# Performance work log

Hardware: AMD Instinct MI355X
Metric: run time of the kernel (lower is better)

The kernel has to match this reference:

```python
import jax, jax.numpy as jnp
import numpy as np

CH = 512


def _maxpool2(t):
    # 2x2 max pool, stride 2, NCHW
    B, C, H, W = t.shape
    return t.reshape(B, C, H // 2, 2, W // 2, 2).max(axis=(3, 5))


def setup_inputs() -> dict:
    key = jax.random.key(0)
    ks = jax.random.split(key, 6)
    B, C, H, W = 8, CH, 64, 64
    x = jax.random.normal(ks[0], (B, C, H, W), dtype=jnp.float32)
    # 1x1 conv weights stored as [out_ch, in_ch]
    w_theta = jax.random.normal(ks[1], (C // 8, C), dtype=jnp.float32) * (1.0 / np.sqrt(C))
    w_phi = jax.random.normal(ks[2], (C // 8, C), dtype=jnp.float32) * (1.0 / np.sqrt(C))
    w_g = jax.random.normal(ks[3], (C // 2, C), dtype=jnp.float32) * (1.0 / np.sqrt(C))
    w_o = jax.random.normal(ks[4], (C, C // 2), dtype=jnp.float32) * (1.0 / np.sqrt(C // 2))
    # gamma is a learned scalar (init 0.0 in the original); use 0.5 so the
    # attention branch contributes to the output for testing purposes.
    gamma = jnp.float32(0.5)
    return {"x": x, "w_theta": w_theta, "w_phi": w_phi, "w_g": w_g, "w_o": w_o, "gamma": gamma}


def reference(x, w_theta, w_phi, w_g, w_o, gamma):
    B, C, H, W = x.shape
    c8, c2 = C // 8, C // 2
    # 1x1 conv projections
    theta = jnp.einsum('bchw,oc->bohw', x, w_theta)           # [B, C/8, H, W]
    phi = _maxpool2(jnp.einsum('bchw,oc->bohw', x, w_phi))    # [B, C/8, H/2, W/2]
    g = _maxpool2(jnp.einsum('bchw,oc->bohw', x, w_g))        # [B, C/2, H/2, W/2]
    n, m = H * W, (H * W) // 4
    theta = theta.reshape(B, c8, n)
    phi = phi.reshape(B, c8, m)
    g = g.reshape(B, c2, m)
    # unscaled attention scores: [B, n, m]
    beta = jax.nn.softmax(jnp.einsum('bcn,bcm->bnm', theta, phi), axis=-1)
    # attend: g @ beta^T -> [B, C/2, n]
    att = jnp.einsum('bcm,bnm->bcn', g, beta).reshape(B, c2, H, W)
    o = jnp.einsum('bchw,oc->bohw', att, w_o)                 # [B, C, H, W]
    return gamma * o + x
```

## Files before the change

kernel.cpp:

```cpp
#include <hip/hip_runtime.h>
#include <math.h>

constexpr int CB = 8;
constexpr int CC = 512;
constexpr int CN = 4096;
constexpr int CM = 1024;
constexpr int C8 = 64;
constexpr int C2 = 256;

typedef __attribute__((ext_vector_type(8))) short short8;
typedef __attribute__((ext_vector_type(8))) _Float16 half8;
typedef __attribute__((ext_vector_type(4))) float f32x4;

__device__ inline unsigned short f2bf(float f) {
  unsigned int u = __float_as_uint(f);
  return (unsigned short)((u + 0x7FFFu + ((u >> 16) & 1u)) >> 16);
}
__device__ inline unsigned short f16bits(float f) {
  union { _Float16 h; unsigned short u; } c;
  c.h = (_Float16)f;
  return c.u;
}

__global__ __launch_bounds__(256)
void conv_w(const float* __restrict__ wt, const float* __restrict__ wp,
            const float* __restrict__ wg, const float* __restrict__ wo,
            _Float16* __restrict__ wth, _Float16* __restrict__ wtl,
            _Float16* __restrict__ wph, _Float16* __restrict__ wpl,
            _Float16* __restrict__ wgf, unsigned short* __restrict__ woh) {
  const int i = blockIdx.x * 256 + threadIdx.x;
  if (i < 32768) {
    float a = wt[i];
    _Float16 h = (_Float16)a;
    wth[i] = h; wtl[i] = (_Float16)(a - (float)h);
    a = wp[i];
    h = (_Float16)a;
    wph[i] = h; wpl[i] = (_Float16)(a - (float)h);
  }
  wgf[i] = (_Float16)wg[i];
  woh[i] = f2bf(wo[i]);
}

__global__ __launch_bounds__(256)
void xpose(const float* __restrict__ X, _Float16* __restrict__ xT) {
  __shared__ __align__(16) float raw[64][68];
  const int b = blockIdx.z, c0 = blockIdx.y * 64, n0 = blockIdx.x * 64;
  const float* Xb = X + ((size_t)b * CC + c0) * CN + n0;
  const int tid = threadIdx.x;
#pragma unroll
  for (int it = 0; it < 4; ++it) {
    const int idx = it * 256 + tid;
    const int row = idx >> 4, col4 = (idx & 15) * 4;
    *(float4*)&raw[row][col4] = *(const float4*)&Xb[(size_t)row * CN + col4];
  }
  __syncthreads();
  unsigned short* Yb = (unsigned short*)(xT + ((size_t)b * CN + n0) * CC + c0);
#pragma unroll
  for (int it = 0; it < 4; ++it) {
    const int idx = it * 256 + tid;
    const int n = idx >> 4, c4 = (idx & 15) * 4;
    ushort4 o;
    o.x = f16bits(raw[c4 + 0][n]);
    o.y = f16bits(raw[c4 + 1][n]);
    o.z = f16bits(raw[c4 + 2][n]);
    o.w = f16bits(raw[c4 + 3][n]);
    *(ushort4*)&Yb[(size_t)n * CC + c4] = o;
  }
}

__global__ __launch_bounds__(256)
void proj_th(const _Float16* __restrict__ Wh, const _Float16* __restrict__ Wl,
             const _Float16* __restrict__ xT, _Float16* __restrict__ thT) {
  __shared__ __align__(16) unsigned short LT[64][68];
  const int b = blockIdx.y, n0 = blockIdx.x * 64;
  const int tid = threadIdx.x;
  const int w = tid >> 6, l = tid & 63;
  const int l15 = l & 15, quad = l >> 4;
  f32x4 acc[4] = {};
  const _Float16* Brow = xT + (size_t)(b * CN + n0 + w * 16 + l15) * CC;
  for (int k0 = 0; k0 < CC; k0 += 32) {
    const half8 bfr = *(const half8*)&Brow[k0 + quad * 8];
#pragma unroll
    for (int i = 0; i < 4; ++i) {
      const half8 ah = *(const half8*)&Wh[(size_t)(i * 16 + l15) * CC + k0 + quad * 8];
      const half8 al = *(const half8*)&Wl[(size_t)(i * 16 + l15) * CC + k0 + quad * 8];
      acc[i] = __builtin_amdgcn_mfma_f32_16x16x32_f16(ah, bfr, acc[i], 0, 0, 0);
      acc[i] = __builtin_amdgcn_mfma_f32_16x16x32_f16(al, bfr, acc[i], 0, 0, 0);
    }
  }
#pragma unroll
  for (int i = 0; i < 4; ++i)
#pragma unroll
    for (int r = 0; r < 4; ++r)
      LT[w * 16 + l15][i * 16 + quad * 4 + r] = f16bits(acc[i][r]);
  __syncthreads();
  unsigned short* Yb = (unsigned short*)(thT + (size_t)(b * CN + n0) * C8);
#pragma unroll
  for (int it = 0; it < 4; ++it) {
    const int idx = it * 256 + tid;
    const int pos = idx >> 4, c4 = (idx & 15) * 4;
    ushort4 v = *(const ushort4*)&LT[pos][c4];
    *(ushort4*)&Yb[(size_t)pos * C8 + c4] = v;
  }
}

__global__ __launch_bounds__(256)
void proj_pg(const _Float16* __restrict__ Wph, const _Float16* __restrict__ Wpl,
             const _Float16* __restrict__ Wg, const _Float16* __restrict__ xT,
             _Float16* __restrict__ phT, unsigned short* __restrict__ gbf) {
  __shared__ float Pbuf[2][64][33];
  const int b = blockIdx.z, mt = blockIdx.y, tile = blockIdx.x;
  const int n0 = tile * 256;
  const int tid = threadIdx.x;
  const int w = tid >> 6, l = tid & 63;
  const int l15 = l & 15, quad = l >> 4;
  const bool isphi = (mt == 0);
  const _Float16* Ah = isphi ? Wph : (Wg + (size_t)(mt - 1) * 64 * CC);
  f32x4 acc[4][4] = {};
  const _Float16* Bbase = xT + (size_t)(b * CN + n0 + w * 64) * CC;
  for (int k0 = 0; k0 < CC; k0 += 32) {
    half8 bf[4], ah[4];
#pragma unroll
    for (int j = 0; j < 4; ++j)
      bf[j] = *(const half8*)&Bbase[(size_t)(j * 16 + l15) * CC + k0 + quad * 8];
#pragma unroll
    for (int i = 0; i < 4; ++i)
      ah[i] = *(const half8*)&Ah[(size_t)(i * 16 + l15) * CC + k0 + quad * 8];
#pragma unroll
    for (int i = 0; i < 4; ++i)
#pragma unroll
      for (int j = 0; j < 4; ++j)
        acc[i][j] = __builtin_amdgcn_mfma_f32_16x16x32_f16(ah[i], bf[j], acc[i][j], 0, 0, 0);
    if (isphi) {
      half8 al[4];
#pragma unroll
      for (int i = 0; i < 4; ++i)
        al[i] = *(const half8*)&Wpl[(size_t)(i * 16 + l15) * CC + k0 + quad * 8];
#pragma unroll
      for (int i = 0; i < 4; ++i)
#pragma unroll
        for (int j = 0; j < 4; ++j)
          acc[i][j] = __builtin_amdgcn_mfma_f32_16x16x32_f16(al[i], bf[j], acc[i][j], 0, 0, 0);
    }
  }
  const bool owner = ((l15 & 1) == 0);
  const int colh = l15 >> 1;
  if (w & 1) {
#pragma unroll
    for (int i = 0; i < 4; ++i)
#pragma unroll
      for (int j = 0; j < 4; ++j)
#pragma unroll
        for (int r = 0; r < 4; ++r) {
          float v = acc[i][j][r];
          float o = __shfl_xor(v, 1);
          v = fmaxf(v, o);
          if (owner) Pbuf[w >> 1][i * 16 + quad * 4 + r][j * 8 + colh] = v;
        }
  }
  __syncthreads();
  if (!(w & 1)) {
    const int pr = tile * 2 + (w >> 1);
    unsigned short* phB = (unsigned short*)(phT + ((size_t)b * CM + pr * 32) * C8);
#pragma unroll
    for (int i = 0; i < 4; ++i)
#pragma unroll
      for (int j = 0; j < 4; ++j)
#pragma unroll
        for (int r = 0; r < 4; ++r) {
          float v = acc[i][j][r];
          float o = __shfl_xor(v, 1);
          v = fmaxf(v, o);
          if (owner) {
            const int oc = i * 16 + quad * 4 + r;
            const int col = j * 8 + colh;
            v = fmaxf(v, Pbuf[w >> 1][oc][col]);
            if (isphi)
              phB[(size_t)col * C8 + oc] = f16bits(v);
            else
              gbf[((size_t)b * C2 + (mt - 1) * 64 + oc) * CM + pr * 32 + col] = f2bf(v);
          }
        }
  }
}

__global__ __launch_bounds__(256)
void attn_v4(const _Float16* __restrict__ thT, const _Float16* __restrict__ phT,
             const unsigned short* __restrict__ gbf,
             unsigned short* __restrict__ attbf) {
  __shared__ __align__(16) unsigned short Pl[2][4][16][40];
  __shared__ float Dinv[64];
  const int b = blockIdx.y;
  const int q0 = blockIdx.x * 64;
  const int tid = threadIdx.x;
  const int w = tid >> 6, l = tid & 63;
  const int l15 = l & 15, quad = l >> 4;
  half8 tb[2];
#pragma unroll
  for (int kc = 0; kc < 2; ++kc)
    tb[kc] = *(const half8*)&thT[(size_t)(b * CN + q0 + w * 16 + l15) * C8 +
                                 kc * 32 + quad * 8];
  f32x4 acc[4][4] = {};
  float dnp = 0.f;
  const _Float16* phB = phT + (size_t)b * CM * C8;
  const unsigned short* gB = gbf + (size_t)b * C2 * CM;

  for (int j0 = 0; j0 < CM; j0 += 32) {
    const int buf = (j0 >> 5) & 1;
    short8 gf[4];
#pragma unroll
    for (int ct = 0; ct < 4; ++ct)
      gf[ct] = *(const short8*)&gB[(size_t)(w * 64 + ct * 16 + l15) * CM +
                                   j0 + quad * 8];
    half8 pa[2][2];
#pragma unroll
    for (int jt = 0; jt < 2; ++jt)
#pragma unroll
      for (int kc = 0; kc < 2; ++kc)
        pa[jt][kc] = *(const half8*)&phB[(size_t)(j0 + jt * 16 + l15) * C8 +
                                         kc * 32 + quad * 8];
    f32x4 S0 = {0.f, 0.f, 0.f, 0.f}, S1 = {0.f, 0.f, 0.f, 0.f};
    S0 = __builtin_amdgcn_mfma_f32_16x16x32_f16(pa[0][0], tb[0], S0, 0, 0, 0);
    S0 = __builtin_amdgcn_mfma_f32_16x16x32_f16(pa[0][1], tb[1], S0, 0, 0, 0);
    S1 = __builtin_amdgcn_mfma_f32_16x16x32_f16(pa[1][0], tb[0], S1, 0, 0, 0);
    S1 = __builtin_amdgcn_mfma_f32_16x16x32_f16(pa[1][1], tb[1], S1, 0, 0, 0);
    float e0[4], e1[4];
#pragma unroll
    for (int r = 0; r < 4; ++r) { e0[r] = __expf(S0[r]); e1[r] = __expf(S1[r]); }
    dnp += (e0[0] + e0[1]) + (e0[2] + e0[3]) +
           (e1[0] + e1[1]) + (e1[2] + e1[3]);
    ushort4 w0, w1;
    w0.x = f2bf(e0[0]); w0.y = f2bf(e0[1]); w0.z = f2bf(e0[2]); w0.w = f2bf(e0[3]);
    w1.x = f2bf(e1[0]); w1.y = f2bf(e1[1]); w1.z = f2bf(e1[2]); w1.w = f2bf(e1[3]);
    *(ushort4*)&Pl[buf][w][l15][quad * 4] = w0;
    *(ushort4*)&Pl[buf][w][l15][16 + quad * 4] = w1;
    __syncthreads();
    short8 pfrag[4];
#pragma unroll
    for (int qs = 0; qs < 4; ++qs)
      pfrag[qs] = *(const short8*)&Pl[buf][qs][l15][quad * 8];
#pragma unroll
    for (int ct = 0; ct < 4; ++ct)
#pragma unroll
      for (int qs = 0; qs < 4; ++qs)
        acc[qs][ct] = __builtin_amdgcn_mfma_f32_16x16x32_bf16(pfrag[qs], gf[ct],
                                                              acc[qs][ct], 0, 0, 0);
  }
  float d = dnp;
  d += __shfl_xor(d, 16);
  d += __shfl_xor(d, 32);
  if (quad == 0) Dinv[w * 16 + l15] = 1.0f / d;
  __syncthreads();
  unsigned short* attB = attbf + (size_t)(b * CN + q0) * C2;
#pragma unroll
  for (int qs = 0; qs < 4; ++qs) {
#pragma unroll
    for (int r = 0; r < 4; ++r) {
      const int row = qs * 16 + quad * 4 + r;
      const float iv = Dinv[row];
#pragma unroll
      for (int ct = 0; ct < 4; ++ct)
        attB[(size_t)row * C2 + w * 64 + ct * 16 + l15] =
            f2bf(acc[qs][ct][r] * iv);
    }
  }
}

__global__ __launch_bounds__(256)
void oproj_mfma(const unsigned short* __restrict__ woh,
                const unsigned short* __restrict__ attbf,
                const float* __restrict__ X, const float* __restrict__ gamma,
                float* __restrict__ out) {
  const int b = blockIdx.z;
  const int mt = blockIdx.y;
  const int n0 = blockIdx.x * 256;
  const int tid = threadIdx.x;
  const int w = tid >> 6, l = tid & 63;
  const int l15 = l & 15, quad = l >> 4;
  const unsigned short* Bb = attbf + (size_t)b * CN * C2;
  f32x4 acc[4][4] = {};
  for (int k0 = 0; k0 < C2; k0 += 32) {
    short8 a[4], bb[4];
#pragma unroll
    for (int i = 0; i < 4; ++i)
      a[i] = *(const short8*)&woh[(size_t)(mt * 64 + i * 16 + l15) * C2 + k0 + quad * 8];
#pragma unroll
    for (int j = 0; j < 4; ++j)
      bb[j] = *(const short8*)&Bb[(size_t)(n0 + w * 64 + j * 16 + l15) * C2 + k0 + quad * 8];
#pragma unroll
    for (int i = 0; i < 4; ++i)
#pragma unroll
      for (int j = 0; j < 4; ++j)
        acc[i][j] = __builtin_amdgcn_mfma_f32_16x16x32_bf16(a[i], bb[j], acc[i][j], 0, 0, 0);
  }
  const float gm = gamma[0];
#pragma unroll
  for (int i = 0; i < 4; ++i)
#pragma unroll
    for (int j = 0; j < 4; ++j)
#pragma unroll
      for (int r = 0; r < 4; ++r) {
        const int c = mt * 64 + i * 16 + quad * 4 + r;
        const int pos = n0 + w * 64 + j * 16 + l15;
        const size_t idx = ((size_t)b * CC + c) * CN + pos;
        out[idx] = X[idx] + gm * acc[i][j][r];
      }
}

extern "C" void kernel_launch(void* const* d_in, const int* in_sizes, int n_in,
                              void* d_out, int out_size, void* d_ws, size_t ws_size,
                              hipStream_t stream) {
  const float* x       = (const float*)d_in[0];
  const float* w_theta = (const float*)d_in[1];
  const float* w_phi   = (const float*)d_in[2];
  const float* w_g     = (const float*)d_in[3];
  const float* w_o     = (const float*)d_in[4];
  const float* gamma   = (const float*)d_in[5];
  float* out = (float*)d_out;
  char* wsb = (char*)d_ws;

  _Float16*       xT    = (_Float16*)(wsb + 0);
  _Float16*       thT   = (_Float16*)(wsb + 33554432);
  _Float16*       phT   = (_Float16*)(wsb + 37748736);
  unsigned short* gbf   = (unsigned short*)(wsb + 38797312);
  _Float16*       wth   = (_Float16*)(wsb + 42991616);
  _Float16*       wtl   = (_Float16*)(wsb + 43057152);
  _Float16*       wph   = (_Float16*)(wsb + 43122688);
  _Float16*       wpl   = (_Float16*)(wsb + 43188224);
  _Float16*       wgf   = (_Float16*)(wsb + 43253760);
  unsigned short* woh   = (unsigned short*)(wsb + 43515904);
  unsigned short* attbf = (unsigned short*)(wsb + 0);

  dim3 blk(256);
  conv_w<<<512, blk, 0, stream>>>(w_theta, w_phi, w_g, w_o,
                                  wth, wtl, wph, wpl, wgf, woh);
  xpose<<<dim3(64, 8, CB), blk, 0, stream>>>(x, xT);
  proj_th<<<dim3(64, CB), blk, 0, stream>>>(wth, wtl, xT, thT);
  proj_pg<<<dim3(16, 5, CB), blk, 0, stream>>>(wph, wpl, wgf, xT, phT, gbf);
  attn_v4<<<dim3(64, CB), blk, 0, stream>>>(thT, phT, gbf, attbf);
  oproj_mfma<<<dim3(16, 8, CB), blk, 0, stream>>>(woh, attbf, x, gamma, out);
}
```

Baseline: 342.9 us.

## Shrink output projection tiles and stage epilogue through LDS for vector stores

```diff
diff --git a/kernel.cpp b/kernel.cpp
--- a/kernel.cpp
+++ b/kernel.cpp
@@ -266,45 +266,62 @@
   }
 }
 
-__global__ __launch_bounds__(256)
-void oproj_mfma(const unsigned short* __restrict__ woh,
-                const unsigned short* __restrict__ attbf,
-                const float* __restrict__ X, const float* __restrict__ gamma,
-                float* __restrict__ out) {
+__global__ __launch_bounds__(256, 8)
+void oproj_v2(const unsigned short* __restrict__ woh,
+              const unsigned short* __restrict__ attbf,
+              const float* __restrict__ X, const float* __restrict__ gamma,
+              float* __restrict__ out) {
+  __shared__ __align__(16) float Tw[4][16][34];
   const int b = blockIdx.z;
   const int mt = blockIdx.y;
-  const int n0 = blockIdx.x * 256;
+  const int n0 = blockIdx.x * 64;
   const int tid = threadIdx.x;
   const int w = tid >> 6, l = tid & 63;
   const int l15 = l & 15, quad = l >> 4;
+  const int wc = w >> 1, wn = w & 1;
+  const int cbase = mt * 64 + wc * 32;
+  const int nbase = n0 + wn * 32;
   const unsigned short* Bb = attbf + (size_t)b * CN * C2;
-  f32x4 acc[4][4] = {};
+  f32x4 acc[2][2] = {};
   for (int k0 = 0; k0 < C2; k0 += 32) {
-    short8 a[4], bb[4];
-#pragma unroll
-    for (int i = 0; i < 4; ++i)
-      a[i] = *(const short8*)&woh[(size_t)(mt * 64 + i * 16 + l15) * C2 + k0 + quad * 8];
-#pragma unroll
-    for (int j = 0; j < 4; ++j)
-      bb[j] = *(const short8*)&Bb[(size_t)(n0 + w * 64 + j * 16 + l15) * C2 + k0 + quad * 8];
-#pragma unroll
-    for (int i = 0; i < 4; ++i)
-#pragma unroll
-      for (int j = 0; j < 4; ++j)
+    short8 a[2], bb[2];
+#pragma unroll
+    for (int i = 0; i < 2; ++i)
+      a[i] = *(const short8*)&woh[(size_t)(cbase + i * 16 + l15) * C2 + k0 + quad * 8];
+#pragma unroll
+    for (int j = 0; j < 2; ++j)
+      bb[j] = *(const short8*)&Bb[(size_t)(nbase + j * 16 + l15) * C2 + k0 + quad * 8];
+#pragma unroll
+    for (int i = 0; i < 2; ++i)
+#pragma unroll
+      for (int j = 0; j < 2; ++j)
         acc[i][j] = __builtin_amdgcn_mfma_f32_16x16x32_bf16(a[i], bb[j], acc[i][j], 0, 0, 0);
   }
   const float gm = gamma[0];
-#pragma unroll
-  for (int i = 0; i < 4; ++i)
-#pragma unroll
-    for (int j = 0; j < 4; ++j)
-#pragma unroll
-      for (int r = 0; r < 4; ++r) {
-        const int c = mt * 64 + i * 16 + quad * 4 + r;
-        const int pos = n0 + w * 64 + j * 16 + l15;
-        const size_t idx = ((size_t)b * CC + c) * CN + pos;
-        out[idx] = X[idx] + gm * acc[i][j][r];
-      }
+  const int cp = l >> 2;
+  const int nq = (l & 3) * 8;
+#pragma unroll
+  for (int i = 0; i < 2; ++i) {
+#pragma unroll
+    for (int j = 0; j < 2; ++j)
+#pragma unroll
+      for (int r = 0; r < 4; ++r)
+        Tw[w][quad * 4 + r][j * 16 + l15] = acc[i][j][r];
+    const float4 v0 = *(const float4*)&Tw[w][cp][nq];
+    const float4 v1 = *(const float4*)&Tw[w][cp][nq + 4];
+    const int c = cbase + i * 16 + cp;
+    const size_t idx = ((size_t)b * CC + c) * CN + nbase + nq;
+    const float4 x0 = *(const float4*)&X[idx];
+    const float4 x1 = *(const float4*)&X[idx + 4];
+    float4 o0, o1;
+    o0.x = x0.x + gm * v0.x; o0.y = x0.y + gm * v0.y;
+    o0.z = x0.z + gm * v0.z; o0.w = x0.w + gm * v0.w;
+    o1.x = x1.x + gm * v1.x; o1.y = x1.y + gm * v1.y;
+    o1.z = x1.z + gm * v1.z; o1.w = x1.w + gm * v1.w;
+    *(float4*)&out[idx] = o0;
+    *(float4*)&out[idx + 4] = o1;
+    __syncthreads();
+  }
 }
 
 extern "C" void kernel_launch(void* const* d_in, const int* in_sizes, int n_in,
@@ -338,5 +355,5 @@
   proj_th<<<dim3(64, CB), blk, 0, stream>>>(wth, wtl, xT, thT);
   proj_pg<<<dim3(16, 5, CB), blk, 0, stream>>>(wph, wpl, wgf, xT, phT, gbf);
   attn_v4<<<dim3(64, CB), blk, 0, stream>>>(thT, phT, gbf, attbf);
-  oproj_mfma<<<dim3(16, 8, CB), blk, 0, stream>>>(woh, attbf, x, gamma, out);
-}
+  oproj_v2<<<dim3(64, 8, CB), blk, 0, stream>>>(woh, attbf, x, gamma, out);
+}
```

Measured after the change: 338.5 us. About the same (-1.3%).
